# Kernel tuning notes

Hardware: AMD Instinct MI355X
Metric: run time of the kernel (lower is better)

The kernel has to match this reference:

```python
import jax, jax.numpy as jnp
import numpy as np

B, N, DIM, H, DH = 2, 2048, 1024, 16, 64
SOFTCAP = 50.0
SCALE = DH ** -0.5
EPS = 1e-12


def _rmsnorm(x, gamma):
    # F.normalize (l2norm over last dim) * sqrt(dim) * (gamma + 1)
    norm = jnp.maximum(jnp.linalg.norm(x, axis=-1, keepdims=True), EPS)
    return (x / norm) * (DIM ** 0.5) * (gamma + 1.0)


def _rotate_half(t):
    # interleaved pairs: (x1, x2) -> (-x2, x1), as in rotary_embedding_torch
    t = t.reshape(*t.shape[:-1], -1, 2)
    x1, x2 = t[..., 0], t[..., 1]
    return jnp.stack((-x2, x1), axis=-1).reshape(*t.shape[:-2], -1)


def _apply_rotary(freqs, t):
    # freqs: [n, d] broadcast over [b, h, n, d]
    return t * jnp.cos(freqs) + _rotate_half(t) * jnp.sin(freqs)


def setup_inputs() -> dict:
    key = jax.random.key(0)
    k0, k1, k2, k3, k4 = jax.random.split(key, 5)
    x = jax.random.normal(k0, (B, N, DIM), jnp.float32)
    gamma = jax.random.normal(k1, (DIM,), jnp.float32) * 0.02
    w_qkv = jax.random.normal(k2, (DIM, 3 * H * DH), jnp.float32) * 0.02
    w_out = jax.random.normal(k3, (H * DH, DIM), jnp.float32) * 0.02
    rotary_emb = jax.random.normal(k4, (N, DH), jnp.float32)
    attn_mask = jnp.broadcast_to(jnp.tril(jnp.ones((N, N), bool)), (B, N, N))
    return {"x": x, "attn_mask": attn_mask, "rotary_emb": rotary_emb,
            "gamma": gamma, "w_qkv": w_qkv, "w_out": w_out}


def reference(x, attn_mask, rotary_emb, gamma, w_qkv, w_out):
    x = _rmsnorm(x, gamma)
    qkv = (x @ w_qkv).reshape(B, N, 3, H, DH)        # b n (qkv h d)
    qkv = jnp.transpose(qkv, (2, 0, 3, 1, 4))        # qkv b h n d
    q, k, v = qkv[0], qkv[1], qkv[2]
    q = _apply_rotary(rotary_emb, q)
    k = _apply_rotary(rotary_emb, k)
    q = q * SCALE
    sim = jnp.einsum('bhid,bhjd->bhij', q, k)
    sim = jnp.tanh(sim / SOFTCAP) * SOFTCAP          # softclamp
    mask_value = -jnp.finfo(sim.dtype).max
    sim = jnp.where(attn_mask[:, None, :, :], sim, mask_value)
    attn = jax.nn.softmax(sim, axis=-1)
    out = jnp.einsum('bhij,bhjd->bhid', attn, v)
    out = jnp.transpose(out, (0, 2, 1, 3)).reshape(B, N, H * DH)  # b n (h d)
    return out @ w_out
```

## Files before the change

### kernel.cpp

```cpp
#include <hip/hip_runtime.h>
#include <hip/hip_bf16.h>

typedef unsigned short u16;
typedef unsigned int u32;
typedef __bf16 bf16x8 __attribute__((ext_vector_type(8)));
typedef float f32x4 __attribute__((ext_vector_type(4)));

#define NB 2
#define NSEQ 2048
#define NDIM 1024
#define NH 16
#define NDH 64

static __device__ __forceinline__ u16 f2bf(float f) {
  return __builtin_bit_cast(u16, (__bf16)f);
}
static __device__ __forceinline__ float bf2f(u16 u) {
  union { u32 u; float f; } a; a.u = ((u32)u) << 16; return a.f;
}
static __device__ __forceinline__ bf16x8 ldbf8(const u16* p) {
  return *(const bf16x8*)p;
}
static __device__ __forceinline__ f32x4 mfma16(bf16x8 a, bf16x8 b, f32x4 c) {
  return __builtin_amdgcn_mfma_f32_16x16x32_bf16(a, b, c, 0, 0, 0);
}
static __device__ __forceinline__ float fexp2(float x) {
  return __builtin_amdgcn_exp2f(x);
}

__global__ __launch_bounds__(256) void k_transpose(const float* __restrict__ in,
                                                   u16* __restrict__ out,
                                                   int R, int C) {
  __shared__ u16 tile[64][65];
  const int r0 = blockIdx.x * 64, c0 = blockIdx.y * 64;
  const int t = threadIdx.x;
  const int tr = t >> 6;
  const int tc = t & 63;
#pragma unroll 4
  for (int p = 0; p < 16; p++) {
    int r = p * 4 + tr;
    tile[r][tc] = f2bf(in[(size_t)(r0 + r) * C + (c0 + tc)]);
  }
  __syncthreads();
#pragma unroll 4
  for (int p = 0; p < 16; p++) {
    int rr = p * 4 + tr;
    out[(size_t)(c0 + rr) * R + (r0 + tc)] = tile[tc][rr];
  }
}

__global__ __launch_bounds__(256) void k_rmsnorm(const float* __restrict__ x,
                                                 const float* __restrict__ gamma,
                                                 u16* __restrict__ xn) {
  __shared__ float part[4];
  const int row = blockIdx.x;
  const int t = threadIdx.x;
  const float4 v = ((const float4*)(x + (size_t)row * NDIM))[t];
  float ss = v.x * v.x + v.y * v.y + v.z * v.z + v.w * v.w;
#pragma unroll
  for (int off = 1; off < 64; off <<= 1) ss += __shfl_xor(ss, off, 64);
  if ((t & 63) == 0) part[t >> 6] = ss;
  __syncthreads();
  const float tot = part[0] + part[1] + part[2] + part[3];
  const float scale = 32.0f / fmaxf(sqrtf(tot), 1e-12f);
  const float4 g = ((const float4*)gamma)[t];
  u16 o0 = f2bf(v.x * scale * (g.x + 1.0f));
  u16 o1 = f2bf(v.y * scale * (g.y + 1.0f));
  u16 o2 = f2bf(v.z * scale * (g.z + 1.0f));
  u16 o3 = f2bf(v.w * scale * (g.w + 1.0f));
  uint2 pv;
  pv.x = (u32)o0 | ((u32)o1 << 16);
  pv.y = (u32)o2 | ((u32)o3 << 16);
  *(uint2*)(xn + (size_t)row * NDIM + t * 4) = pv;
}

template <int EPI>
__global__ __launch_bounds__(256) void k_gemm_bt(const u16* __restrict__ A,
                                                 const u16* __restrict__ BT,
                                                 float* __restrict__ Of,
                                                 u16* __restrict__ O0,
                                                 u16* __restrict__ O1,
                                                 u16* __restrict__ O2) {
  constexpr int KD = 1024, NT = KD / 32;
  __shared__ u16 As[128][40];
  __shared__ u16 Bs[128][40];
  const int m0 = blockIdx.x * 128, n0 = blockIdx.y * 128;
  const int t = threadIdx.x;
  const int w = t >> 6, l = t & 63, lo = l & 15, hi = l >> 4;
  const int wr = (w >> 1) * 64, wc = (w & 1) * 64;
  const int ar = t >> 1, ac = (t & 1) * 16;
  f32x4 acc[4][4] = {};
  const u16* ag = A + (size_t)(m0 + ar) * KD + ac;
  const u16* bg = BT + (size_t)(n0 + ar) * KD + ac;
  uint4 av0 = *(const uint4*)(ag);
  uint4 av1 = *(const uint4*)(ag + 8);
  uint4 bv0 = *(const uint4*)(bg);
  uint4 bv1 = *(const uint4*)(bg + 8);
  for (int kt = 0; kt < NT; kt++) {
    __syncthreads();
    *(uint4*)&As[ar][ac] = av0; *(uint4*)&As[ar][ac + 8] = av1;
    *(uint4*)&Bs[ar][ac] = bv0; *(uint4*)&Bs[ar][ac + 8] = bv1;
    __syncthreads();
    if (kt + 1 < NT) {
      const int k0 = (kt + 1) * 32;
      av0 = *(const uint4*)(ag + k0);
      av1 = *(const uint4*)(ag + k0 + 8);
      bv0 = *(const uint4*)(bg + k0);
      bv1 = *(const uint4*)(bg + k0 + 8);
    }
    bf16x8 af[4], bb[4];
#pragma unroll
    for (int i = 0; i < 4; i++) af[i] = ldbf8(&As[wr + i * 16 + lo][hi * 8]);
#pragma unroll
    for (int i = 0; i < 4; i++) bb[i] = ldbf8(&Bs[wc + i * 16 + lo][hi * 8]);
#pragma unroll
    for (int i = 0; i < 4; i++)
#pragma unroll
      for (int j = 0; j < 4; j++)
        acc[i][j] = mfma16(af[i], bb[j], acc[i][j]);
  }
#pragma unroll
  for (int i = 0; i < 4; i++) {
#pragma unroll
    for (int j = 0; j < 4; j++) {
      const int gr0 = m0 + wr + i * 16 + hi * 4;
      const int gc = n0 + wc + j * 16 + lo;
#pragma unroll
      for (int r = 0; r < 4; r++) {
        const int row = gr0 + r;
        if (EPI == 0) {
          Of[(size_t)row * 1024 + gc] = acc[i][j][r];
        } else {
          const u16 bv = f2bf(acc[i][j][r]);
          const int which = gc >> 10, rem = gc & 1023;
          const int h = rem >> 6, dh = rem & 63;
          const int b = row >> 11, ns = row & 2047;
          if (which == 2) {
            O2[(((size_t)b * NH + h) * NDH + dh) * NSEQ + ns] = bv;
          } else {
            const size_t idx = ((((size_t)b * NH + h) * NSEQ) + ns) * NDH + dh;
            (which == 0 ? O0 : O1)[idx] = bv;
          }
        }
      }
    }
  }
}

__global__ __launch_bounds__(256) void k_rotary(u16* __restrict__ qb,
                                                u16* __restrict__ kb,
                                                const float* __restrict__ rot) {
  const int gi = blockIdx.x * 256 + threadIdx.x;
  const int half = gi >> 19;
  const int i = gi & ((1 << 19) - 1);
  u16* buf = half ? kb : qb;
  const float scale = half ? 1.0f : 0.125f;
  const int d0 = (i & 7) * 8;
  const int n = (i >> 3) & (NSEQ - 1);
  union { uint4 v; u16 s[8]; } u;
  u.v = *(const uint4*)(buf + (size_t)i * 8);
  float fr[8];
  *(float4*)&fr[0] = *(const float4*)(rot + n * NDH + d0);
  *(float4*)&fr[4] = *(const float4*)(rot + n * NDH + d0 + 4);
  union { uint4 v; u16 s[8]; } o;
#pragma unroll
  for (int p = 0; p < 4; p++) {
    float a = bf2f(u.s[2 * p]), b = bf2f(u.s[2 * p + 1]);
    float s0, c0, s1, c1;
    __sincosf(fr[2 * p], &s0, &c0);
    __sincosf(fr[2 * p + 1], &s1, &c1);
    o.s[2 * p] = f2bf((a * c0 - b * s0) * scale);
    o.s[2 * p + 1] = f2bf((b * c1 + a * s1) * scale);
  }
  *(uint4*)(buf + (size_t)i * 8) = o.v;
}

#define KCH(row, ch) ((((ch) ^ ((row) & 7)) * 8))
__global__ __launch_bounds__(128) void k_attn(const u16* __restrict__ Q,
                                              const u16* __restrict__ K,
                                              const u16* __restrict__ Vt,
                                              u16* __restrict__ O) {
  __shared__ u16 Ks[64][64];
  __shared__ u16 Vs[64][64];
  __shared__ u16 Ps[2][16][64];
  const int qt = 63 - (blockIdx.x >> 5);
  const int bh = blockIdx.x & 31;
  const int b = bh >> 4, h = bh & 15;
  const size_t base = (size_t)bh * (NSEQ * NDH);
  const int t = threadIdx.x;
  const int w = t >> 6, l = t & 63, lo = l & 15, hi = l >> 4;
  const int q0 = qt * 32;

  bf16x8 aq0, aq1;
  {
    const u16* qp = Q + base + (size_t)(q0 + w * 16 + lo) * NDH;
    aq0 = ldbf8(qp + hi * 8);
    aq1 = ldbf8(qp + 32 + hi * 8);
  }
  f32x4 accO[4] = {};
  float l_part[4] = {0.f, 0.f, 0.f, 0.f};

  const int sr = t >> 1;
  const int sh = (t & 1) * 4;
  const u16* kg = K + base + (size_t)sr * NDH;
  const u16* vg = Vt + ((size_t)bh * NDH + sr) * NSEQ;
  const int nkt = (qt >> 1) + 1;
  const int ktd = qt >> 1;
  const int rowg = q0 + w * 16 + hi * 4;

  for (int kt = 0; kt < nkt; kt++) {
    __syncthreads();
    {
      const u16* kp = kg + (size_t)kt * 64 * NDH;
      const u16* vp = vg + kt * 64;
#pragma unroll
      for (int j = 0; j < 4; j++) {
        const int c = sh + j;
        *(uint4*)&Ks[sr][KCH(sr, c)] = *(const uint4*)(kp + c * 8);
        *(uint4*)&Vs[sr][KCH(sr, c)] = *(const uint4*)(vp + c * 8);
      }
    }
    __syncthreads();

    f32x4 s[4];
#pragma unroll
    for (int nt = 0; nt < 4; nt++) {
      const int kr = nt * 16 + lo;
      f32x4 z = {};
      z = mfma16(aq0, ldbf8(&Ks[kr][KCH(kr, hi)]), z);
      z = mfma16(aq1, ldbf8(&Ks[kr][KCH(kr, 4 + hi)]), z);
      s[nt] = z;
    }
    const bool diag = (kt == ktd);
#pragma unroll
    for (int nt = 0; nt < 4; nt++) {
      const int col = kt * 64 + nt * 16 + lo;
#pragma unroll
      for (int r = 0; r < 4; r++) {
        const float v = s[nt][r];
        const float wv = fexp2(v * 0.0577078016f);
        const float ex = fmaf(__builtin_amdgcn_rcpf(wv + 1.0f),
                              -144.2695040889f, 72.1347520444f);
        float p = fexp2(ex);
        if (diag && col > rowg + r) p = 0.0f;
        s[nt][r] = p;
        l_part[r] += p;
      }
    }
#pragma unroll
    for (int nt = 0; nt < 4; nt++)
#pragma unroll
      for (int r = 0; r < 4; r++) {
        const int row = hi * 4 + r;
        Ps[w][row][KCH(row, 2 * nt + (lo >> 3)) + (lo & 7)] = f2bf(s[nt][r]);
      }

    const bf16x8 ap0 = ldbf8(&Ps[w][lo][KCH(lo, hi)]);
    const bf16x8 ap1 = ldbf8(&Ps[w][lo][KCH(lo, 4 + hi)]);
#pragma unroll
    for (int dt = 0; dt < 4; dt++) {
      const int d = dt * 16 + lo;
      accO[dt] = mfma16(ap0, ldbf8(&Vs[d][KCH(d, hi)]), accO[dt]);
      accO[dt] = mfma16(ap1, ldbf8(&Vs[d][KCH(d, 4 + hi)]), accO[dt]);
    }
  }
  float lr[4];
#pragma unroll
  for (int r = 0; r < 4; r++) {
    float lv = l_part[r];
    lv += __shfl_xor(lv, 1, 64);
    lv += __shfl_xor(lv, 2, 64);
    lv += __shfl_xor(lv, 4, 64);
    lv += __shfl_xor(lv, 8, 64);
    lr[r] = __builtin_amdgcn_rcpf(lv);
  }
#pragma unroll
  for (int dt = 0; dt < 4; dt++) {
#pragma unroll
    for (int r = 0; r < 4; r++) {
      const int row = rowg + r;
      const float v = accO[dt][r] * lr[r];
      const size_t idx = (((size_t)(b * NSEQ + row)) * NH + h) * NDH + dt * 16 + lo;
      O[idx] = f2bf(v);
    }
  }
}

extern "C" void kernel_launch(void* const* d_in, const int* in_sizes, int n_in,
                              void* d_out, int out_size, void* d_ws, size_t ws_size,
                              hipStream_t stream) {
  const float* x     = (const float*)d_in[0];
  const float* rot   = (const float*)d_in[2];
  const float* gamma = (const float*)d_in[3];
  const float* wqkv  = (const float*)d_in[4];
  const float* wout  = (const float*)d_in[5];

  char* ws = (char*)d_ws;
  u16* xn    = (u16*)(ws);
  u16* wqkvT = (u16*)(ws + (size_t)( 8u << 20));
  u16* woutT = (u16*)(ws + (size_t)(14u << 20));
  u16* qb    = (u16*)(ws + (size_t)(16u << 20));
  u16* kb    = (u16*)(ws + (size_t)(24u << 20));
  u16* vt    = (u16*)(ws + (size_t)(32u << 20));
  u16* ob    = xn;

  k_transpose<<<dim3(16, 48), 256, 0, stream>>>(wqkv, wqkvT, 1024, 3072);
  k_transpose<<<dim3(16, 16), 256, 0, stream>>>(wout, woutT, 1024, 1024);
  k_rmsnorm<<<4096, 256, 0, stream>>>(x, gamma, xn);
  k_gemm_bt<1><<<dim3(32, 24), 256, 0, stream>>>(xn, wqkvT, nullptr, qb, kb, vt);
  k_rotary<<<4096, 256, 0, stream>>>(qb, kb, rot);
  k_attn<<<2048, 128, 0, stream>>>(qb, kb, vt, ob);
  k_gemm_bt<0><<<dim3(32, 8), 256, 0, stream>>>(ob, woutT, (float*)d_out, nullptr, nullptr, nullptr);
}
```

Baseline: 149.5 us.

## Use direct global-to-LDS loads in GEMM and pair causal query tiles in attention

The GEMM now uses a K-tile of 64 and loads it with global_load_lds straight into an XOR-swizzled shared layout. This replaces the register-staged prefetch, and each wave then issues two MFMAs per fragment pair. The attention kernel now gives each block two query tiles (pr and 63-pr) so causal work is balanced across blocks, and the launch drops to 1024 blocks. In exchange, the GEMM loses its overlap of the next tile's global loads with compute, and each attention block runs longer serially.

```diff
diff --git a/kernel.cpp b/kernel.cpp
--- a/kernel.cpp
+++ b/kernel.cpp
@@ -27,6 +27,9 @@
 static __device__ __forceinline__ float fexp2(float x) {
   return __builtin_amdgcn_exp2f(x);
 }
+#define GLDS(g, d) __builtin_amdgcn_global_load_lds(                         \
+    (const __attribute__((address_space(1))) void*)(g),                      \
+    (__attribute__((address_space(3))) void*)(d), 16, 0, 0)
 
 __global__ __launch_bounds__(256) void k_transpose(const float* __restrict__ in,
                                                    u16* __restrict__ out,
@@ -81,43 +84,46 @@
                                                  u16* __restrict__ O0,
                                                  u16* __restrict__ O1,
                                                  u16* __restrict__ O2) {
-  constexpr int KD = 1024, NT = KD / 32;
-  __shared__ u16 As[128][40];
-  __shared__ u16 Bs[128][40];
+  constexpr int KD = 1024, BK = 64, NT = KD / BK;
+  __shared__ u16 As[128 * BK];
+  __shared__ u16 Bs[128 * BK];
   const int m0 = blockIdx.x * 128, n0 = blockIdx.y * 128;
   const int t = threadIdx.x;
   const int w = t >> 6, l = t & 63, lo = l & 15, hi = l >> 4;
   const int wr = (w >> 1) * 64, wc = (w & 1) * 64;
-  const int ar = t >> 1, ac = (t & 1) * 16;
+  const int srow = w * 32 + (l >> 3);
+  const int sch  = (l & 7) ^ (l >> 3);
+  const u16* ag = A  + (size_t)(m0 + srow) * KD + sch * 8;
+  const u16* bg = BT + (size_t)(n0 + srow) * KD + sch * 8;
+  u16* asd = As + w * 2048;
+  u16* bsd = Bs + w * 2048;
   f32x4 acc[4][4] = {};
-  const u16* ag = A + (size_t)(m0 + ar) * KD + ac;
-  const u16* bg = BT + (size_t)(n0 + ar) * KD + ac;
-  uint4 av0 = *(const uint4*)(ag);
-  uint4 av1 = *(const uint4*)(ag + 8);
-  uint4 bv0 = *(const uint4*)(bg);
-  uint4 bv1 = *(const uint4*)(bg + 8);
   for (int kt = 0; kt < NT; kt++) {
+    const int k0 = kt * BK;
     __syncthreads();
-    *(uint4*)&As[ar][ac] = av0; *(uint4*)&As[ar][ac + 8] = av1;
-    *(uint4*)&Bs[ar][ac] = bv0; *(uint4*)&Bs[ar][ac + 8] = bv1;
+#pragma unroll
+    for (int i = 0; i < 4; i++) {
+      GLDS(ag + k0 + i * 8 * KD, asd + i * 512);
+      GLDS(bg + k0 + i * 8 * KD, bsd + i * 512);
+    }
     __syncthreads();
-    if (kt + 1 < NT) {
-      const int k0 = (kt + 1) * 32;
-      av0 = *(const uint4*)(ag + k0);
-      av1 = *(const uint4*)(ag + k0 + 8);
-      bv0 = *(const uint4*)(bg + k0);
-      bv1 = *(const uint4*)(bg + k0 + 8);
-    }
-    bf16x8 af[4], bb[4];
-#pragma unroll
-    for (int i = 0; i < 4; i++) af[i] = ldbf8(&As[wr + i * 16 + lo][hi * 8]);
-#pragma unroll
-    for (int i = 0; i < 4; i++) bb[i] = ldbf8(&Bs[wc + i * 16 + lo][hi * 8]);
+    bf16x8 af[4][2], bb[4][2];
+#pragma unroll
+    for (int i = 0; i < 4; i++) {
+      const int Ra = wr + i * 16 + lo, xa = Ra & 7;
+      af[i][0] = ldbf8(&As[Ra * 64 + ((hi ^ xa) << 3)]);
+      af[i][1] = ldbf8(&As[Ra * 64 + (((4 + hi) ^ xa) << 3)]);
+      const int Rb = wc + i * 16 + lo, xb = Rb & 7;
+      bb[i][0] = ldbf8(&Bs[Rb * 64 + ((hi ^ xb) << 3)]);
+      bb[i][1] = ldbf8(&Bs[Rb * 64 + (((4 + hi) ^ xb) << 3)]);
+    }
 #pragma unroll
     for (int i = 0; i < 4; i++)
 #pragma unroll
-      for (int j = 0; j < 4; j++)
-        acc[i][j] = mfma16(af[i], bb[j], acc[i][j]);
+      for (int j = 0; j < 4; j++) {
+        acc[i][j] = mfma16(af[i][0], bb[j][0], acc[i][j]);
+        acc[i][j] = mfma16(af[i][1], bb[j][1], acc[i][j]);
+      }
   }
 #pragma unroll
   for (int i = 0; i < 4; i++) {
@@ -183,105 +189,109 @@
   __shared__ u16 Ks[64][64];
   __shared__ u16 Vs[64][64];
   __shared__ u16 Ps[2][16][64];
-  const int qt = 63 - (blockIdx.x >> 5);
+  const int pr = blockIdx.x >> 5;
   const int bh = blockIdx.x & 31;
   const int b = bh >> 4, h = bh & 15;
   const size_t base = (size_t)bh * (NSEQ * NDH);
   const int t = threadIdx.x;
   const int w = t >> 6, l = t & 63, lo = l & 15, hi = l >> 4;
-  const int q0 = qt * 32;
-
-  bf16x8 aq0, aq1;
-  {
-    const u16* qp = Q + base + (size_t)(q0 + w * 16 + lo) * NDH;
-    aq0 = ldbf8(qp + hi * 8);
-    aq1 = ldbf8(qp + 32 + hi * 8);
-  }
-  f32x4 accO[4] = {};
-  float l_part[4] = {0.f, 0.f, 0.f, 0.f};
 
   const int sr = t >> 1;
   const int sh = (t & 1) * 4;
   const u16* kg = K + base + (size_t)sr * NDH;
   const u16* vg = Vt + ((size_t)bh * NDH + sr) * NSEQ;
-  const int nkt = (qt >> 1) + 1;
-  const int ktd = qt >> 1;
-  const int rowg = q0 + w * 16 + hi * 4;
-
-  for (int kt = 0; kt < nkt; kt++) {
-    __syncthreads();
+
+#pragma unroll
+  for (int half = 0; half < 2; half++) {
+    const int qt = half ? (63 - pr) : pr;
+    const int q0 = qt * 32;
+    bf16x8 aq0, aq1;
     {
-      const u16* kp = kg + (size_t)kt * 64 * NDH;
-      const u16* vp = vg + kt * 64;
-#pragma unroll
-      for (int j = 0; j < 4; j++) {
-        const int c = sh + j;
-        *(uint4*)&Ks[sr][KCH(sr, c)] = *(const uint4*)(kp + c * 8);
-        *(uint4*)&Vs[sr][KCH(sr, c)] = *(const uint4*)(vp + c * 8);
-      }
-    }
-    __syncthreads();
-
-    f32x4 s[4];
-#pragma unroll
-    for (int nt = 0; nt < 4; nt++) {
-      const int kr = nt * 16 + lo;
-      f32x4 z = {};
-      z = mfma16(aq0, ldbf8(&Ks[kr][KCH(kr, hi)]), z);
-      z = mfma16(aq1, ldbf8(&Ks[kr][KCH(kr, 4 + hi)]), z);
-      s[nt] = z;
-    }
-    const bool diag = (kt == ktd);
-#pragma unroll
-    for (int nt = 0; nt < 4; nt++) {
-      const int col = kt * 64 + nt * 16 + lo;
+      const u16* qp = Q + base + (size_t)(q0 + w * 16 + lo) * NDH;
+      aq0 = ldbf8(qp + hi * 8);
+      aq1 = ldbf8(qp + 32 + hi * 8);
+    }
+    f32x4 accO[4] = {};
+    float l_part[4] = {0.f, 0.f, 0.f, 0.f};
+    const int nkt = (qt >> 1) + 1;
+    const int ktd = qt >> 1;
+    const int rowg = q0 + w * 16 + hi * 4;
+
+    for (int kt = 0; kt < nkt; kt++) {
+      __syncthreads();
+      {
+        const u16* kp = kg + (size_t)kt * 64 * NDH;
+        const u16* vp = vg + kt * 64;
+#pragma unroll
+        for (int j = 0; j < 4; j++) {
+          const int c = sh + j;
+          *(uint4*)&Ks[sr][KCH(sr, c)] = *(const uint4*)(kp + c * 8);
+          *(uint4*)&Vs[sr][KCH(sr, c)] = *(const uint4*)(vp + c * 8);
+        }
+      }
+      __syncthreads();
+
+      f32x4 s[4];
+#pragma unroll
+      for (int nt = 0; nt < 4; nt++) {
+        const int kr = nt * 16 + lo;
+        f32x4 z = {};
+        z = mfma16(aq0, ldbf8(&Ks[kr][KCH(kr, hi)]), z);
+        z = mfma16(aq1, ldbf8(&Ks[kr][KCH(kr, 4 + hi)]), z);
+        s[nt] = z;
+      }
+      const bool diag = (kt == ktd);
+#pragma unroll
+      for (int nt = 0; nt < 4; nt++) {
+        const int col = kt * 64 + nt * 16 + lo;
+#pragma unroll
+        for (int r = 0; r < 4; r++) {
+          const float v = s[nt][r];
+          const float wv = fexp2(v * 0.0577078016f);
+          const float ex = fmaf(__builtin_amdgcn_rcpf(wv + 1.0f),
+                                -144.2695040889f, 72.1347520444f);
+          float p = fexp2(ex);
+          if (diag && col > rowg + r) p = 0.0f;
+          s[nt][r] = p;
+          l_part[r] += p;
+        }
+      }
+#pragma unroll
+      for (int nt = 0; nt < 4; nt++)
+#pragma unroll
+        for (int r = 0; r < 4; r++) {
+          const int row = hi * 4 + r;
+          Ps[w][row][KCH(row, 2 * nt + (lo >> 3)) + (lo & 7)] = f2bf(s[nt][r]);
+        }
+
+      const bf16x8 ap0 = ldbf8(&Ps[w][lo][KCH(lo, hi)]);
+      const bf16x8 ap1 = ldbf8(&Ps[w][lo][KCH(lo, 4 + hi)]);
+#pragma unroll
+      for (int dt = 0; dt < 4; dt++) {
+        const int d = dt * 16 + lo;
+        accO[dt] = mfma16(ap0, ldbf8(&Vs[d][KCH(d, hi)]), accO[dt]);
+        accO[dt] = mfma16(ap1, ldbf8(&Vs[d][KCH(d, 4 + hi)]), accO[dt]);
+      }
+    }
+    float lr[4];
+#pragma unroll
+    for (int r = 0; r < 4; r++) {
+      float lv = l_part[r];
+      lv += __shfl_xor(lv, 1, 64);
+      lv += __shfl_xor(lv, 2, 64);
+      lv += __shfl_xor(lv, 4, 64);
+      lv += __shfl_xor(lv, 8, 64);
+      lr[r] = __builtin_amdgcn_rcpf(lv);
+    }
+#pragma unroll
+    for (int dt = 0; dt < 4; dt++) {
 #pragma unroll
       for (int r = 0; r < 4; r++) {
-        const float v = s[nt][r];
-        const float wv = fexp2(v * 0.0577078016f);
-        const float ex = fmaf(__builtin_amdgcn_rcpf(wv + 1.0f),
-                              -144.2695040889f, 72.1347520444f);
-        float p = fexp2(ex);
-        if (diag && col > rowg + r) p = 0.0f;
-        s[nt][r] = p;
-        l_part[r] += p;
-      }
-    }
-#pragma unroll
-    for (int nt = 0; nt < 4; nt++)
-#pragma unroll
-      for (int r = 0; r < 4; r++) {
-        const int row = hi * 4 + r;
-        Ps[w][row][KCH(row, 2 * nt + (lo >> 3)) + (lo & 7)] = f2bf(s[nt][r]);
-      }
-
-    const bf16x8 ap0 = ldbf8(&Ps[w][lo][KCH(lo, hi)]);
-    const bf16x8 ap1 = ldbf8(&Ps[w][lo][KCH(lo, 4 + hi)]);
-#pragma unroll
-    for (int dt = 0; dt < 4; dt++) {
-      const int d = dt * 16 + lo;
-      accO[dt] = mfma16(ap0, ldbf8(&Vs[d][KCH(d, hi)]), accO[dt]);
-      accO[dt] = mfma16(ap1, ldbf8(&Vs[d][KCH(d, 4 + hi)]), accO[dt]);
-    }
-  }
-  float lr[4];
-#pragma unroll
-  for (int r = 0; r < 4; r++) {
-    float lv = l_part[r];
-    lv += __shfl_xor(lv, 1, 64);
-    lv += __shfl_xor(lv, 2, 64);
-    lv += __shfl_xor(lv, 4, 64);
-    lv += __shfl_xor(lv, 8, 64);
-    lr[r] = __builtin_amdgcn_rcpf(lv);
-  }
-#pragma unroll
-  for (int dt = 0; dt < 4; dt++) {
-#pragma unroll
-    for (int r = 0; r < 4; r++) {
-      const int row = rowg + r;
-      const float v = accO[dt][r] * lr[r];
-      const size_t idx = (((size_t)(b * NSEQ + row)) * NH + h) * NDH + dt * 16 + lo;
-      O[idx] = f2bf(v);
+        const int row = rowg + r;
+        const float v = accO[dt][r] * lr[r];
+        const size_t idx = (((size_t)(b * NSEQ + row)) * NH + h) * NDH + dt * 16 + lo;
+        O[idx] = f2bf(v);
+      }
     }
   }
 }
@@ -309,6 +319,6 @@
   k_rmsnorm<<<4096, 256, 0, stream>>>(x, gamma, xn);
   k_gemm_bt<1><<<dim3(32, 24), 256, 0, stream>>>(xn, wqkvT, nullptr, qb, kb, vt);
   k_rotary<<<4096, 256, 0, stream>>>(qb, kb, rot);
-  k_attn<<<2048, 128, 0, stream>>>(qb, kb, vt, ob);
+  k_attn<<<1024, 128, 0, stream>>>(qb, kb, vt, ob);
   k_gemm_bt<0><<<dim3(32, 8), 256, 0, stream>>>(ob, woutT, (float*)d_out, nullptr, nullptr, nullptr);
 }
```

Result: faster. 139.9 us (-6.4%).
